# Kernel optimization log

Hardware: AMD Instinct MI355X
Metric: run time of the kernel (lower is better)

The kernel has to match this reference:

```python
import jax, jax.numpy as jnp
import numpy as np

NUM_HEADS = 16


def setup_inputs() -> dict:
    key = jax.random.key(0)
    ks = jax.random.split(key, 8)
    B, L, Hd = 2, 2048, 1024
    s = 0.02
    return {
        "x": jax.random.normal(ks[0], (B, L, Hd), jnp.float32),
        "y": jax.random.normal(ks[1], (B, L, Hd), jnp.float32),
        "mask": jnp.zeros((B, L), jnp.bool_),  # True = padding (masked out)
        "Wq_w": jax.random.normal(ks[2], (Hd, Hd), jnp.float32) * s,
        "Wq_b": jnp.zeros((Hd,), jnp.float32),
        "Wkv_w": jax.random.normal(ks[3], (Hd, 2 * Hd), jnp.float32) * s,
        "Wkv_b": jnp.zeros((2 * Hd,), jnp.float32),
        "proj_w": jax.random.normal(ks[4], (Hd, Hd), jnp.float32) * s,
        "proj_b": jnp.zeros((Hd,), jnp.float32),
    }


def reference(x, y, mask, Wq_w, Wq_b, Wkv_w, Wkv_b, proj_w, proj_b):
    B, L, Hd = x.shape
    H = NUM_HEADS
    D = Hd // H
    scale = 1.0 / np.sqrt(D)

    # projections (torch Linear: stored here already as (in, out))
    q = (x @ Wq_w + Wq_b).reshape(B, L, H, D).transpose(0, 2, 1, 3)   # bhld
    kv = (y @ Wkv_w + Wkv_b).reshape(B, L, 2, H, D)
    k = kv[:, :, 0].transpose(0, 2, 1, 3)                             # bhkd
    v = kv[:, :, 1].transpose(0, 2, 1, 3)                             # bhkd

    attn = jnp.einsum("bhld,bhkd->bhlk", q, k) * scale

    # combined padding (over keys) + causal mask; True = masked
    causal = jnp.triu(jnp.ones((L, L), jnp.bool_), 1)                 # (L, L)
    combined = mask[:, None, None, :] | causal[None, None]            # (B,1,L,L)
    attn = jnp.where(combined, -jnp.inf, attn)

    p = jax.nn.softmax(attn, axis=-1)
    out = jnp.einsum("bhlk,bhkd->bhld", p, v)
    out = out.transpose(0, 2, 1, 3).reshape(B, L, Hd)
    return out @ proj_w + proj_b
```

## Files before the change

kernel.cpp:

```cpp
#include <hip/hip_runtime.h>
#include <stdint.h>

#define B_  2
#define L_  2048
#define HD_ 1024
#define H_  16
#define D_  64

typedef unsigned short u16;
typedef __attribute__((ext_vector_type(8))) short bf16x8;
typedef __attribute__((ext_vector_type(4))) float f32x4;

#define MFMA16(a, b, c) __builtin_amdgcn_mfma_f32_16x16x32_bf16((a), (b), (c), 0, 0, 0)

__device__ __forceinline__ void gload16(const void* g, void* l) {
  __builtin_amdgcn_global_load_lds((const __attribute__((address_space(1))) void*)g,
                                   (__attribute__((address_space(3))) void*)l, 16, 0, 0);
}

__device__ __forceinline__ u16 f2bf(float f) {
  union { float f; uint32_t u; } c; c.f = f;
  uint32_t u = c.u + 0x7FFFu + ((c.u >> 16) & 1u);
  return (u16)(u >> 16);
}

__device__ __forceinline__ float bf2f(u16 v) {
  union { uint32_t u; float f; } c; c.u = (uint32_t)v << 16;
  return c.f;
}

__device__ __forceinline__ uint32_t cvt_pk_bf16(float lo, float hi) {
  uint32_t r;
  asm("v_cvt_pk_bf16_f32 %0, %1, %2" : "=v"(r) : "v"(lo), "v"(hi));
  return r;
}

__global__ void prologue_k(const float* __restrict__ x, const float* __restrict__ y,
                           u16* __restrict__ xb, u16* __restrict__ yb,
                           const float* __restrict__ Wq, const float* __restrict__ Wkv,
                           const float* __restrict__ Wp,
                           u16* __restrict__ Wqt, u16* __restrict__ Wkvt,
                           u16* __restrict__ Wpt) {
  int bid = blockIdx.x;
  int t = threadIdx.x;
  if (bid < 4096) {
    const float* in = bid < 2048 ? x : y;
    u16* out = bid < 2048 ? xb : yb;
    int i = ((bid & 2047) * 256 + t) * 8;
    float4 a = *(const float4*)(in + i);
    float4 b = *(const float4*)(in + i + 4);
    bf16x8 r;
    r[0] = (short)f2bf(a.x); r[1] = (short)f2bf(a.y); r[2] = (short)f2bf(a.z); r[3] = (short)f2bf(a.w);
    r[4] = (short)f2bf(b.x); r[5] = (short)f2bf(b.y); r[6] = (short)f2bf(b.z); r[7] = (short)f2bf(b.w);
    *(bf16x8*)(out + i) = r;
    return;
  }
  int f = bid - 4096;
  const float* src; u16* dst; int Nfull, bx, by;
  if (f < 1024)      { src = Wq;  dst = Wqt;  Nfull = 1024; bx = f & 31;  by = f >> 5; }
  else if (f < 3072) { int g2 = f - 1024; src = Wkv; dst = Wkvt; Nfull = 2048; bx = g2 & 63; by = g2 >> 6; }
  else               { int g2 = f - 3072; src = Wp;  dst = Wpt;  Nfull = 1024; bx = g2 & 31; by = g2 >> 5; }
  __shared__ float tile[32][33];
  int tc = t & 31, tr = t >> 5;
  int nb = bx * 32, kb = by * 32;
#pragma unroll
  for (int i = 0; i < 4; i++)
    tile[tr + i * 8][tc] = src[(size_t)(kb + tr + i * 8) * Nfull + nb + tc];
  __syncthreads();
#pragma unroll
  for (int i = 0; i < 4; i++) {
    int nl = tr + i * 8;
    dst[(size_t)(nb + nl) * 1024 + kb + tc] = f2bf(tile[tc][nl]);
  }
}

__device__ __forceinline__ void gemm64_body(
    char* sA, char* sB,
    const u16* __restrict__ A, const u16* __restrict__ Bt,
    const float* __restrict__ bias, void* __restrict__ outp,
    int N, int epi, int bm, int bn)
{
  int t = threadIdx.x;
  int lane = t & 63, w = t >> 6;
  int g = lane >> 4, l15 = lane & 15;
  int wr = w >> 1, wc = w & 1;

  f32x4 zero = {0.f, 0.f, 0.f, 0.f};
  f32x4 acc[2][4];
#pragma unroll
  for (int mi = 0; mi < 2; mi++)
#pragma unroll
    for (int ni = 0; ni < 4; ni++) acc[mi][ni] = zero;

#define GSTAGE64(bufi, k0s) do {                                                        \
    _Pragma("unroll")                                                                   \
    for (int it = 0; it < 2; it++) {             \
      int c = it * 256 + t;                                                             \
      int r = c >> 3, sp = c & 7;                                                       \
      int off = (sp ^ (r & 7)) << 4;                                                    \
      gload16((const char*)(A + (size_t)(bm + r) * 1024 + (k0s)) + off,                 \
              sA + (bufi) * 8192 + c * 16);                                             \
    }                                                                                   \
    _Pragma("unroll")                                                                   \
    for (int it = 0; it < 4; it++) {           \
      int c = it * 256 + t;                                                             \
      int r = c >> 3, sp = c & 7;                                                       \
      int off = (sp ^ (r & 7)) << 4;                                                    \
      gload16((const char*)(Bt + (size_t)(bn + r) * 1024 + (k0s)) + off,                \
              sB + (bufi) * 16384 + c * 16);                                            \
    } } while (0)

  GSTAGE64(0, 0);
  int buf = 0;
#pragma unroll 1
  for (int kt = 0; kt < 16; kt++) {
    __builtin_amdgcn_sched_barrier(0);
    __builtin_amdgcn_s_barrier();
    if (kt < 15) {
      GSTAGE64(buf ^ 1, (kt + 1) << 6);
      asm volatile("s_waitcnt vmcnt(6)" ::: "memory");
    } else {
      asm volatile("s_waitcnt vmcnt(0)" ::: "memory");
    }
    __builtin_amdgcn_s_barrier();
    __builtin_amdgcn_sched_barrier(0);

    const char* cA = sA + buf * 8192;
    const char* cB = sB + buf * 16384;
#pragma unroll
    for (int kc = 0; kc < 2; kc++) {
      bf16x8 af[2], bfr[4];
#pragma unroll
      for (int mi = 0; mi < 2; mi++) {
        int r = wr * 32 + mi * 16 + l15;
        af[mi] = *(const bf16x8*)(cA + r * 128 + (((kc * 4 + g) ^ (r & 7)) << 4));
      }
#pragma unroll
      for (int ni = 0; ni < 4; ni++) {
        int r = wc * 64 + ni * 16 + l15;
        bfr[ni] = *(const bf16x8*)(cB + r * 128 + (((kc * 4 + g) ^ (r & 7)) << 4));
      }
#pragma unroll
      for (int mi = 0; mi < 2; mi++)
#pragma unroll
        for (int ni = 0; ni < 4; ni++)
          acc[mi][ni] = MFMA16(af[mi], bfr[ni], acc[mi][ni]);
    }
    buf ^= 1;
  }
#undef GSTAGE64

  float bv[4];
#pragma unroll
  for (int ni = 0; ni < 4; ni++) bv[ni] = bias[bn + wc * 64 + ni * 16 + l15];

  if (epi == 2) {
    float* fo = (float*)outp;
#pragma unroll
    for (int mi = 0; mi < 2; mi++)
#pragma unroll
      for (int ni = 0; ni < 4; ni++) {
        int n = bn + wc * 64 + ni * 16 + l15;
#pragma unroll
        for (int r = 0; r < 4; r++) {
          int m = bm + wr * 32 + mi * 16 + g * 4 + r;
          fo[(size_t)m * N + n] = acc[mi][ni][r] + bv[ni];
        }
      }
  } else {
    const float QS = (epi == 0) ? 0.125f * 1.44269504089f : 1.0f;
    u16* ob = (u16*)outp;
#pragma unroll
    for (int mi = 0; mi < 2; mi++)
#pragma unroll
      for (int ni = 0; ni < 4; ni++) {
        int n = bn + wc * 64 + ni * 16 + l15;
        int kv = n >> 10;
        int hh = (n >> 6) & 15;
        int dd = n & 63;
        int m0 = bm + wr * 32 + mi * 16 + g * 4;
        int bb = m0 >> 11, lq0 = m0 & 2047;
        if (epi == 1 && kv == 1) {
          ushort4 pk;
          pk.x = f2bf(acc[mi][ni][0] + bv[ni]);
          pk.y = f2bf(acc[mi][ni][1] + bv[ni]);
          pk.z = f2bf(acc[mi][ni][2] + bv[ni]);
          pk.w = f2bf(acc[mi][ni][3] + bv[ni]);
          size_t idx = (size_t)(B_ * H_ * L_ * D_) +
                       (((size_t)(bb * H_ + hh) * D_ + dd) * L_ + lq0);
          *(ushort4*)(ob + idx) = pk;
        } else {
#pragma unroll
          for (int r = 0; r < 4; r++) {
            size_t idx = (((size_t)(bb * H_ + hh) * L_ + lq0 + r) * D_) + dd;
            ob[idx] = f2bf((acc[mi][ni][r] + bv[ni]) * QS);
          }
        }
      }
  }
}

__global__ __launch_bounds__(256, 3) void qkv_k(
    const u16* __restrict__ xb, const u16* __restrict__ yb,
    const u16* __restrict__ Wqt, const u16* __restrict__ Wkvt,
    const float* __restrict__ Wq_b, const float* __restrict__ Wkv_b,
    u16* __restrict__ Qout, u16* __restrict__ KVout)
{
  __shared__ char sA[2 * 8192];
  __shared__ char sB[2 * 16384];
  int bx = blockIdx.x, bm = blockIdx.y * 64;
  if (bx < 16)
    gemm64_body(sA, sB, yb, Wkvt, Wkv_b, (void*)KVout, 2048, 1, bm, bx * 128);
  else
    gemm64_body(sA, sB, xb, Wqt, Wq_b, (void*)Qout, 1024, 0, bm, (bx - 16) * 128);
}

__global__ __launch_bounds__(256, 3) void proj_k(
    const u16* __restrict__ A, const u16* __restrict__ Bt,
    const float* __restrict__ bias, float* __restrict__ fo)
{
  __shared__ char sA[2 * 8192];
  __shared__ char sB[2 * 16384];
  gemm64_body(sA, sB, A, Bt, bias, (void*)fo, 1024, 2,
              blockIdx.y * 64, blockIdx.x * 128);
}

__global__ __launch_bounds__(512, 2) void attn_k(
    const u16* __restrict__ Qb, const u16* __restrict__ Kb, const u16* __restrict__ Vt,
    const unsigned char* __restrict__ pad, u16* __restrict__ Ob,
    u16* __restrict__ Opart, float* __restrict__ mlbuf)
{
  __shared__ char sK[3][8192];
  __shared__ char sV[3][8192];
  __shared__ char sP[8][2048];
  int t = threadIdx.x, lane = t & 63, w = t >> 6, g = lane >> 4, l15 = lane & 15;
  int x = blockIdx.x, h = blockIdx.y, b = blockIdx.z, bh = b * H_ + h;
  int role = x >> 3, xp = x & 7;
  int qbH = 15 - xp, qbL = xp;
  int nktH = 2 * qbH + 2;
  const int SPLIT = 17;

  const u16* Kbh = Kb + (size_t)bh * L_ * D_;
  const u16* Vbh = Vt + (size_t)bh * D_ * L_;
  const unsigned char* pdb = pad + b * L_;
  int psw = l15 & 7;

  const uint4* pp = (const uint4*)pdb;
  uint4 pv0 = pp[lane];
  uint4 pv1 = pp[64 + lane];
  uint32_t nzp = pv0.x | pv0.y | pv0.z | pv0.w | pv1.x | pv1.y | pv1.z | pv1.w;
  bool anyp = __ballot(nzp != 0) != 0;

  int srr = t >> 3, ssp = t & 7;
  int sso = (ssp ^ (srr & 7)) << 4;
#define STAGE(bufi, kt0s) do {                                                        \
    gload16((const char*)(Kbh + (size_t)((kt0s) + srr) * D_) + sso, sK[bufi] + t * 16); \
    gload16((const char*)(Vbh + (size_t)srr * L_ + (kt0s)) + sso, sV[bufi] + t * 16);   \
  } while (0)

  int nphase = role ? 1 : 2;
#pragma unroll 1
  for (int ph = 0; ph < nphase; ph++) {
    int qb, lo, hi, mode;
    if (role) { qb = qbH; lo = 0;     hi = SPLIT;     mode = 1; }
    else if (ph == 0) { qb = qbL; lo = 0; hi = 2 * qbL + 2; mode = 0; }
    else { qb = qbH; lo = SPLIT; hi = nktH; mode = 2; }

    int qw0 = qb * 128 + w * 16;
    int bound = qw0 + 15;

    const u16* qp = Qb + ((size_t)bh * L_ + qw0 + l15) * D_ + g * 8;
    bf16x8 qf0 = *(const bf16x8*)qp;
    bf16x8 qf1 = *(const bf16x8*)(qp + 32);

    f32x4 zero = {0.f, 0.f, 0.f, 0.f};
    f32x4 oacc[4];
#pragma unroll
    for (int db = 0; db < 4; db++) oacc[db] = zero;
    float mrun = -1e30f, lrun = 0.f;

    if (ph) __syncthreads();
    STAGE(0, lo << 6);
    int cb = 0, nb = 1;

#pragma unroll 1
    for (int kt = lo; kt < hi; kt++) {
      int kt0 = kt << 6;
      __builtin_amdgcn_sched_barrier(0);
      if (kt + 1 < hi) {
        STAGE(nb, (kt + 1) << 6);
        asm volatile("s_waitcnt vmcnt(2)" ::: "memory");
      } else {
        asm volatile("s_waitcnt vmcnt(0)" ::: "memory");
      }
      __builtin_amdgcn_s_barrier();
      __builtin_amdgcn_sched_barrier(0);

      if (kt0 <= bound) {
        float sc[4][4];
#pragma unroll
        for (int s = 0; s < 4; s++) {
          int kb = kt0 + s * 16;
          bool live = (kb <= bound);
          f32x4 st = zero;
          uint32_t pb = 0;
          if (live) {
            int R = s * 16 + l15, sw = l15 & 7;
            bf16x8 kf0 = *(const bf16x8*)(sK[cb] + R * 128 + ((g ^ sw) << 4));
            bf16x8 kf1 = *(const bf16x8*)(sK[cb] + R * 128 + (((4 + g) ^ sw) << 4));
            st = MFMA16(kf0, qf0, st);
            st = MFMA16(kf1, qf1, st);
            if (anyp) pb = *(const uint32_t*)(pdb + kb + 4 * g);
          }
          bool needm = !live || (kb + 15 > qw0) || anyp;
          if (needm) {
#pragma unroll
            for (int r = 0; r < 4; r++) {
              int key = kb + 4 * g + r;
              bool pm = (pb >> (8 * r)) & 0xffu;
              bool msk = !live || pm || (key > qw0 + l15);
              sc[s][r] = msk ? -1e30f : st[r];
            }
          } else {
#pragma unroll
            for (int r = 0; r < 4; r++) sc[s][r] = st[r];
          }
        }

        float m0 = fmaxf(fmaxf(sc[0][0], sc[0][1]), fmaxf(sc[0][2], sc[0][3]));
        float m1 = fmaxf(fmaxf(sc[1][0], sc[1][1]), fmaxf(sc[1][2], sc[1][3]));
        float m2 = fmaxf(fmaxf(sc[2][0], sc[2][1]), fmaxf(sc[2][2], sc[2][3]));
        float m3 = fmaxf(fmaxf(sc[3][0], sc[3][1]), fmaxf(sc[3][2], sc[3][3]));
        float mt = fmaxf(fmaxf(m0, m1), fmaxf(m2, m3));
        mt = fmaxf(mt, __shfl_xor(mt, 16));
        mt = fmaxf(mt, __shfl_xor(mt, 32));
        if (!__all(mt <= mrun + 8.0f)) {
          float mnew = fmaxf(mrun, mt);
          float al = __builtin_amdgcn_exp2f(mrun - mnew);
          mrun = mnew;
          lrun *= al;
#pragma unroll
          for (int db = 0; db < 4; db++)
#pragma unroll
            for (int r = 0; r < 4; r++) oacc[db][r] *= al;
        }
        float rs = 0.f;
        char* pwb = sP[w] + l15 * 128 + (g & 1) * 8;
#pragma unroll
        for (int s = 0; s < 4; s++) {
          float p0 = __builtin_amdgcn_exp2f(sc[s][0] - mrun);
          float p1 = __builtin_amdgcn_exp2f(sc[s][1] - mrun);
          float p2 = __builtin_amdgcn_exp2f(sc[s][2] - mrun);
          float p3 = __builtin_amdgcn_exp2f(sc[s][3] - mrun);
          rs += (p0 + p1) + (p2 + p3);
          uint32_t w0 = cvt_pk_bf16(p0, p1), w1 = cvt_pk_bf16(p2, p3);
          char* dst = pwb + (((2 * s + (g >> 1)) ^ psw) << 4);
          *(uint32_t*)dst = w0;
          *(uint32_t*)(dst + 4) = w1;
        }
        rs += __shfl_xor(rs, 16);
        rs += __shfl_xor(rs, 32);
        lrun += rs;

#pragma unroll
        for (int kc = 0; kc < 2; kc++) {
          if (kt0 + 32 * kc <= bound) {
            bf16x8 pf = *(const bf16x8*)(sP[w] + l15 * 128 + (((4 * kc + g) ^ psw) << 4));
#pragma unroll
            for (int db = 0; db < 4; db++) {
              int dR = db * 16 + l15;
              bf16x8 vf = *(const bf16x8*)(sV[cb] + dR * 128 +
                                           (((4 * kc + g) ^ (dR & 7)) << 4));
              oacc[db] = MFMA16(vf, pf, oacc[db]);
            }
          }
        }
      }
      cb = (cb == 2) ? 0 : cb + 1;
      nb = (nb == 2) ? 0 : nb + 1;
    }

    float rl = (lrun != 0.f) ? 1.0f / lrun : 0.f;
    int q = qw0 + l15;
    if (mode == 0) {
      u16* op = Ob + ((size_t)b * L_ + q) * HD_ + h * D_ + g * 4;
#pragma unroll
      for (int db = 0; db < 4; db++) {
        ushort4 pk;
        pk.x = f2bf(oacc[db][0] * rl);
        pk.y = f2bf(oacc[db][1] * rl);
        pk.z = f2bf(oacc[db][2] * rl);
        pk.w = f2bf(oacc[db][3] * rl);
        *(ushort4*)(op + db * 16) = pk;
      }
    } else {
      int part = mode - 1;
      size_t prow = (size_t)part * 32768 + (size_t)bh * 1024 + (q - 1024);
      u16* op = Opart + prow * 64 + g * 4;
#pragma unroll
      for (int db = 0; db < 4; db++) {
        ushort4 pk;
        pk.x = f2bf(oacc[db][0] * rl);
        pk.y = f2bf(oacc[db][1] * rl);
        pk.z = f2bf(oacc[db][2] * rl);
        pk.w = f2bf(oacc[db][3] * rl);
        *(ushort4*)(op + db * 16) = pk;
      }
      if (g == 0) {
        mlbuf[prow * 2]     = mrun;
        mlbuf[prow * 2 + 1] = lrun;
      }
    }
  }
#undef STAGE
}

__global__ __launch_bounds__(256) void merge_k(
    const u16* __restrict__ Op, const float* __restrict__ ml, u16* __restrict__ Ob)
{
  int tid = blockIdx.x * 256 + threadIdx.x;
  int d0 = (tid & 7) * 8;
  int row = tid >> 3;
  int qrel = row & 1023, bh = row >> 10;
  int b = bh >> 4, h = bh & 15;
  float m0 = ml[(size_t)row * 2],            l0 = ml[(size_t)row * 2 + 1];
  float m1 = ml[((size_t)32768 + row) * 2],  l1 = ml[((size_t)32768 + row) * 2 + 1];
  float M = fmaxf(m0, m1);
  float w0 = l0 * __builtin_amdgcn_exp2f(m0 - M);
  float w1 = l1 * __builtin_amdgcn_exp2f(m1 - M);
  float rw = 1.0f / (w0 + w1);
  w0 *= rw; w1 *= rw;
  bf16x8 a = *(const bf16x8*)(Op + (size_t)row * 64 + d0);
  bf16x8 c = *(const bf16x8*)(Op + ((size_t)32768 + row) * 64 + d0);
  bf16x8 o;
#pragma unroll
  for (int j = 0; j < 8; j++)
    o[j] = (short)f2bf(w0 * bf2f((u16)a[j]) + w1 * bf2f((u16)c[j]));
  *(bf16x8*)(Ob + ((size_t)b * L_ + 1024 + qrel) * HD_ + h * D_ + d0) = o;
}

extern "C" void kernel_launch(void* const* d_in, const int* in_sizes, int n_in,
                              void* d_out, int out_size, void* d_ws, size_t ws_size,
                              hipStream_t stream) {
  const float* x      = (const float*)d_in[0];
  const float* y      = (const float*)d_in[1];
  const unsigned char* mask = (const unsigned char*)d_in[2];
  const float* Wq_w   = (const float*)d_in[3];
  const float* Wq_b   = (const float*)d_in[4];
  const float* Wkv_w  = (const float*)d_in[5];
  const float* Wkv_b  = (const float*)d_in[6];
  const float* proj_w = (const float*)d_in[7];
  const float* proj_b = (const float*)d_in[8];

  char* ws = (char*)d_ws;
  u16* xb   = (u16*)(ws);
  u16* yb   = (u16*)(ws + (size_t)(8  << 20));
  u16* Wqt  = (u16*)(ws + (size_t)(16 << 20));
  u16* Wkvt = (u16*)(ws + (size_t)(18 << 20));
  u16* Wpt  = (u16*)(ws + (size_t)(22 << 20));
  u16* Qb   = (u16*)(ws + (size_t)(24 << 20));
  u16* Kb   = (u16*)(ws + (size_t)(32 << 20));
  u16* Vtb  = (u16*)(ws + (size_t)(40 << 20));
  u16* Ob   = xb;
  u16* Opart  = yb;
  float* mlbuf = (float*)Wqt;

  hipLaunchKernelGGL(prologue_k, dim3(8192), dim3(256), 0, stream,
                     x, y, xb, yb, Wq_w, Wkv_w, proj_w, Wqt, Wkvt, Wpt);
  hipLaunchKernelGGL(qkv_k, dim3(24, 64), dim3(256), 0, stream,
                     xb, yb, Wqt, Wkvt, Wq_b, Wkv_b, Qb, Kb);
  hipLaunchKernelGGL(attn_k, dim3(16, H_, B_), dim3(512), 0, stream,
                     Qb, Kb, Vtb, mask, Ob, Opart, mlbuf);
  hipLaunchKernelGGL(merge_k, dim3(1024), dim3(256), 0, stream, Opart, mlbuf, Ob);
  hipLaunchKernelGGL(proj_k, dim3(8, 64), dim3(256), 0, stream, Ob, Wpt, proj_b, (float*)d_out);
}
```

Baseline: 114.6 us.

## Fuse attention phases into one pipelined loop and widen weight transpose tiles

The attention kernel's two-phase loop (low q-block, then high q-block tail) becomes a single 17-iteration stream of K/V tiles. The prefetch pipeline therefore continues across the phase boundary, with an in-loop switch that writes the first output and reloads Q. This removes the pipeline drain, the extra barrier and the restaging at the phase change. Separately, the weight transpose in the prologue moves to 64x64 tiles with float4 loads and ushort4 stores, cutting the block count and widening memory accesses, at the cost of more shared memory per block.

```diff
diff --git a/kernel.cpp b/kernel.cpp
--- a/kernel.cpp
+++ b/kernel.cpp
@@ -57,20 +57,30 @@
   }
   int f = bid - 4096;
   const float* src; u16* dst; int Nfull, bx, by;
-  if (f < 1024)      { src = Wq;  dst = Wqt;  Nfull = 1024; bx = f & 31;  by = f >> 5; }
-  else if (f < 3072) { int g2 = f - 1024; src = Wkv; dst = Wkvt; Nfull = 2048; bx = g2 & 63; by = g2 >> 6; }
-  else               { int g2 = f - 3072; src = Wp;  dst = Wpt;  Nfull = 1024; bx = g2 & 31; by = g2 >> 5; }
-  __shared__ float tile[32][33];
-  int tc = t & 31, tr = t >> 5;
-  int nb = bx * 32, kb = by * 32;
-#pragma unroll
-  for (int i = 0; i < 4; i++)
-    tile[tr + i * 8][tc] = src[(size_t)(kb + tr + i * 8) * Nfull + nb + tc];
+  if (f < 256)      { src = Wq;  dst = Wqt;  Nfull = 1024; bx = f & 15;  by = f >> 4; }
+  else if (f < 768) { int g2 = f - 256; src = Wkv; dst = Wkvt; Nfull = 2048; bx = g2 & 31; by = g2 >> 5; }
+  else              { int g2 = f - 768; src = Wp;  dst = Wpt;  Nfull = 1024; bx = g2 & 15; by = g2 >> 4; }
+  __shared__ float tile[64][65];
+  int c = t & 15, r = t >> 4;
+  int nb = bx * 64, kb = by * 64;
+#pragma unroll
+  for (int i = 0; i < 4; i++) {
+    float4 v = *(const float4*)(src + (size_t)(kb + r + i * 16) * Nfull + nb + c * 4);
+    tile[r + i * 16][c * 4 + 0] = v.x;
+    tile[r + i * 16][c * 4 + 1] = v.y;
+    tile[r + i * 16][c * 4 + 2] = v.z;
+    tile[r + i * 16][c * 4 + 3] = v.w;
+  }
   __syncthreads();
 #pragma unroll
   for (int i = 0; i < 4; i++) {
-    int nl = tr + i * 8;
-    dst[(size_t)(nb + nl) * 1024 + kb + tc] = f2bf(tile[tc][nl]);
+    int nl = r + i * 16;
+    ushort4 o;
+    o.x = f2bf(tile[c * 4 + 0][nl]);
+    o.y = f2bf(tile[c * 4 + 1][nl]);
+    o.z = f2bf(tile[c * 4 + 2][nl]);
+    o.w = f2bf(tile[c * 4 + 3][nl]);
+    *(ushort4*)(dst + (size_t)(nb + nl) * 1024 + kb + c * 4) = o;
   }
 }
 
@@ -237,8 +247,9 @@
   int x = blockIdx.x, h = blockIdx.y, b = blockIdx.z, bh = b * H_ + h;
   int role = x >> 3, xp = x & 7;
   int qbH = 15 - xp, qbL = xp;
-  int nktH = 2 * qbH + 2;
   const int SPLIT = 17;
+  int nL = 2 * qbL + 2;
+  int boundary = role ? 99 : nL;
 
   const u16* Kbh = Kb + (size_t)bh * L_ * D_;
   const u16* Vbh = Vt + (size_t)bh * D_ * L_;
@@ -257,162 +268,166 @@
     gload16((const char*)(Kbh + (size_t)((kt0s) + srr) * D_) + sso, sK[bufi] + t * 16); \
     gload16((const char*)(Vbh + (size_t)srr * L_ + (kt0s)) + sso, sV[bufi] + t * 16);   \
   } while (0)
-
-  int nphase = role ? 1 : 2;
+#define KT0_OF(jj) ((role ? (jj) : ((jj) < nL ? (jj) : SPLIT + (jj) - nL)) << 6)
+
+  int qb_cur = role ? qbH : qbL;
+  int qw0 = qb_cur * 128 + w * 16;
+  int bound = qw0 + 15;
+
+  const u16* qp = Qb + ((size_t)bh * L_ + qw0 + l15) * D_ + g * 8;
+  bf16x8 qf0 = *(const bf16x8*)qp;
+  bf16x8 qf1 = *(const bf16x8*)(qp + 32);
+
+  f32x4 zero = {0.f, 0.f, 0.f, 0.f};
+  f32x4 oacc[4];
+#pragma unroll
+  for (int db = 0; db < 4; db++) oacc[db] = zero;
+  float mrun = -1e30f, lrun = 0.f;
+
+  STAGE(0, 0);
+  int cb = 0, nb = 1;
+
 #pragma unroll 1
-  for (int ph = 0; ph < nphase; ph++) {
-    int qb, lo, hi, mode;
-    if (role) { qb = qbH; lo = 0;     hi = SPLIT;     mode = 1; }
-    else if (ph == 0) { qb = qbL; lo = 0; hi = 2 * qbL + 2; mode = 0; }
-    else { qb = qbH; lo = SPLIT; hi = nktH; mode = 2; }
-
-    int qw0 = qb * 128 + w * 16;
-    int bound = qw0 + 15;
-
-    const u16* qp = Qb + ((size_t)bh * L_ + qw0 + l15) * D_ + g * 8;
-    bf16x8 qf0 = *(const bf16x8*)qp;
-    bf16x8 qf1 = *(const bf16x8*)(qp + 32);
-
-    f32x4 zero = {0.f, 0.f, 0.f, 0.f};
-    f32x4 oacc[4];
-#pragma unroll
-    for (int db = 0; db < 4; db++) oacc[db] = zero;
-    float mrun = -1e30f, lrun = 0.f;
-
-    if (ph) __syncthreads();
-    STAGE(0, lo << 6);
-    int cb = 0, nb = 1;
-
-#pragma unroll 1
-    for (int kt = lo; kt < hi; kt++) {
-      int kt0 = kt << 6;
-      __builtin_amdgcn_sched_barrier(0);
-      if (kt + 1 < hi) {
-        STAGE(nb, (kt + 1) << 6);
-        asm volatile("s_waitcnt vmcnt(2)" ::: "memory");
-      } else {
-        asm volatile("s_waitcnt vmcnt(0)" ::: "memory");
-      }
-      __builtin_amdgcn_s_barrier();
-      __builtin_amdgcn_sched_barrier(0);
-
-      if (kt0 <= bound) {
-        float sc[4][4];
-#pragma unroll
-        for (int s = 0; s < 4; s++) {
-          int kb = kt0 + s * 16;
-          bool live = (kb <= bound);
-          f32x4 st = zero;
-          uint32_t pb = 0;
-          if (live) {
-            int R = s * 16 + l15, sw = l15 & 7;
-            bf16x8 kf0 = *(const bf16x8*)(sK[cb] + R * 128 + ((g ^ sw) << 4));
-            bf16x8 kf1 = *(const bf16x8*)(sK[cb] + R * 128 + (((4 + g) ^ sw) << 4));
-            st = MFMA16(kf0, qf0, st);
-            st = MFMA16(kf1, qf1, st);
-            if (anyp) pb = *(const uint32_t*)(pdb + kb + 4 * g);
+  for (int j = 0; j < 17; j++) {
+    __builtin_amdgcn_sched_barrier(0);
+    if (j + 1 < 17) {
+      STAGE(nb, KT0_OF(j + 1));
+      asm volatile("s_waitcnt vmcnt(2)" ::: "memory");
+    } else {
+      asm volatile("s_waitcnt vmcnt(0)" ::: "memory");
+    }
+    __builtin_amdgcn_s_barrier();
+    __builtin_amdgcn_sched_barrier(0);
+
+    if (j == boundary) {
+      float rl0 = (lrun != 0.f) ? 1.0f / lrun : 0.f;
+      int q0 = qw0 + l15;
+      u16* op0 = Ob + ((size_t)b * L_ + q0) * HD_ + h * D_ + g * 4;
+#pragma unroll
+      for (int db = 0; db < 4; db++) {
+        ushort4 pk;
+        pk.x = f2bf(oacc[db][0] * rl0);
+        pk.y = f2bf(oacc[db][1] * rl0);
+        pk.z = f2bf(oacc[db][2] * rl0);
+        pk.w = f2bf(oacc[db][3] * rl0);
+        *(ushort4*)(op0 + db * 16) = pk;
+      }
+      qb_cur = qbH;
+      qw0 = qb_cur * 128 + w * 16;
+      bound = qw0 + 15;
+      const u16* qp2 = Qb + ((size_t)bh * L_ + qw0 + l15) * D_ + g * 8;
+      qf0 = *(const bf16x8*)qp2;
+      qf1 = *(const bf16x8*)(qp2 + 32);
+#pragma unroll
+      for (int db = 0; db < 4; db++) oacc[db] = zero;
+      mrun = -1e30f; lrun = 0.f;
+    }
+
+    int kt0 = KT0_OF(j);
+    if (kt0 <= bound) {
+      float sc[4][4];
+#pragma unroll
+      for (int s = 0; s < 4; s++) {
+        int kb = kt0 + s * 16;
+        bool live = (kb <= bound);
+        f32x4 st = zero;
+        uint32_t pb = 0;
+        if (live) {
+          int R = s * 16 + l15, sw = l15 & 7;
+          bf16x8 kf0 = *(const bf16x8*)(sK[cb] + R * 128 + ((g ^ sw) << 4));
+          bf16x8 kf1 = *(const bf16x8*)(sK[cb] + R * 128 + (((4 + g) ^ sw) << 4));
+          st = MFMA16(kf0, qf0, st);
+          st = MFMA16(kf1, qf1, st);
+          if (anyp) pb = *(const uint32_t*)(pdb + kb + 4 * g);
+        }
+        bool needm = !live || (kb + 15 > qw0) || anyp;
+        if (needm) {
+#pragma unroll
+          for (int r = 0; r < 4; r++) {
+            int key = kb + 4 * g + r;
+            bool pm = (pb >> (8 * r)) & 0xffu;
+            bool msk = !live || pm || (key > qw0 + l15);
+            sc[s][r] = msk ? -1e30f : st[r];
           }
-          bool needm = !live || (kb + 15 > qw0) || anyp;
-          if (needm) {
-#pragma unroll
-            for (int r = 0; r < 4; r++) {
-              int key = kb + 4 * g + r;
-              bool pm = (pb >> (8 * r)) & 0xffu;
-              bool msk = !live || pm || (key > qw0 + l15);
-              sc[s][r] = msk ? -1e30f : st[r];
-            }
-          } else {
-#pragma unroll
-            for (int r = 0; r < 4; r++) sc[s][r] = st[r];
+        } else {
+#pragma unroll
+          for (int r = 0; r < 4; r++) sc[s][r] = st[r];
+        }
+      }
+
+      float m0 = fmaxf(fmaxf(sc[0][0], sc[0][1]), fmaxf(sc[0][2], sc[0][3]));
+      float m1 = fmaxf(fmaxf(sc[1][0], sc[1][1]), fmaxf(sc[1][2], sc[1][3]));
+      float m2 = fmaxf(fmaxf(sc[2][0], sc[2][1]), fmaxf(sc[2][2], sc[2][3]));
+      float m3 = fmaxf(fmaxf(sc[3][0], sc[3][1]), fmaxf(sc[3][2], sc[3][3]));
+      float mt = fmaxf(fmaxf(m0, m1), fmaxf(m2, m3));
+      mt = fmaxf(mt, __shfl_xor(mt, 16));
+      mt = fmaxf(mt, __shfl_xor(mt, 32));
+      if (!__all(mt <= mrun + 8.0f)) {
+        float mnew = fmaxf(mrun, mt);
+        float al = __builtin_amdgcn_exp2f(mrun - mnew);
+        mrun = mnew;
+        lrun *= al;
+#pragma unroll
+        for (int db = 0; db < 4; db++)
+#pragma unroll
+          for (int r = 0; r < 4; r++) oacc[db][r] *= al;
+      }
+      float rs = 0.f;
+      char* pwb = sP[w] + l15 * 128 + (g & 1) * 8;
+#pragma unroll
+      for (int s = 0; s < 4; s++) {
+        float p0 = __builtin_amdgcn_exp2f(sc[s][0] - mrun);
+        float p1 = __builtin_amdgcn_exp2f(sc[s][1] - mrun);
+        float p2 = __builtin_amdgcn_exp2f(sc[s][2] - mrun);
+        float p3 = __builtin_amdgcn_exp2f(sc[s][3] - mrun);
+        rs += (p0 + p1) + (p2 + p3);
+        uint32_t w0 = cvt_pk_bf16(p0, p1), w1 = cvt_pk_bf16(p2, p3);
+        char* dst = pwb + (((2 * s + (g >> 1)) ^ psw) << 4);
+        *(uint32_t*)dst = w0;
+        *(uint32_t*)(dst + 4) = w1;
+      }
+      rs += __shfl_xor(rs, 16);
+      rs += __shfl_xor(rs, 32);
+      lrun += rs;
+
+#pragma unroll
+      for (int kc = 0; kc < 2; kc++) {
+        if (kt0 + 32 * kc <= bound) {
+          bf16x8 pf = *(const bf16x8*)(sP[w] + l15 * 128 + (((4 * kc + g) ^ psw) << 4));
+#pragma unroll
+          for (int db = 0; db < 4; db++) {
+            int dR = db * 16 + l15;
+            bf16x8 vf = *(const bf16x8*)(sV[cb] + dR * 128 +
+                                         (((4 * kc + g) ^ (dR & 7)) << 4));
+            oacc[db] = MFMA16(vf, pf, oacc[db]);
           }
         }
-
-        float m0 = fmaxf(fmaxf(sc[0][0], sc[0][1]), fmaxf(sc[0][2], sc[0][3]));
-        float m1 = fmaxf(fmaxf(sc[1][0], sc[1][1]), fmaxf(sc[1][2], sc[1][3]));
-        float m2 = fmaxf(fmaxf(sc[2][0], sc[2][1]), fmaxf(sc[2][2], sc[2][3]));
-        float m3 = fmaxf(fmaxf(sc[3][0], sc[3][1]), fmaxf(sc[3][2], sc[3][3]));
-        float mt = fmaxf(fmaxf(m0, m1), fmaxf(m2, m3));
-        mt = fmaxf(mt, __shfl_xor(mt, 16));
-        mt = fmaxf(mt, __shfl_xor(mt, 32));
-        if (!__all(mt <= mrun + 8.0f)) {
-          float mnew = fmaxf(mrun, mt);
-          float al = __builtin_amdgcn_exp2f(mrun - mnew);
-          mrun = mnew;
-          lrun *= al;
-#pragma unroll
-          for (int db = 0; db < 4; db++)
-#pragma unroll
-            for (int r = 0; r < 4; r++) oacc[db][r] *= al;
-        }
-        float rs = 0.f;
-        char* pwb = sP[w] + l15 * 128 + (g & 1) * 8;
-#pragma unroll
-        for (int s = 0; s < 4; s++) {
-          float p0 = __builtin_amdgcn_exp2f(sc[s][0] - mrun);
-          float p1 = __builtin_amdgcn_exp2f(sc[s][1] - mrun);
-          float p2 = __builtin_amdgcn_exp2f(sc[s][2] - mrun);
-          float p3 = __builtin_amdgcn_exp2f(sc[s][3] - mrun);
-          rs += (p0 + p1) + (p2 + p3);
-          uint32_t w0 = cvt_pk_bf16(p0, p1), w1 = cvt_pk_bf16(p2, p3);
-          char* dst = pwb + (((2 * s + (g >> 1)) ^ psw) << 4);
-          *(uint32_t*)dst = w0;
-          *(uint32_t*)(dst + 4) = w1;
-        }
-        rs += __shfl_xor(rs, 16);
-        rs += __shfl_xor(rs, 32);
-        lrun += rs;
-
-#pragma unroll
-        for (int kc = 0; kc < 2; kc++) {
-          if (kt0 + 32 * kc <= bound) {
-            bf16x8 pf = *(const bf16x8*)(sP[w] + l15 * 128 + (((4 * kc + g) ^ psw) << 4));
-#pragma unroll
-            for (int db = 0; db < 4; db++) {
-              int dR = db * 16 + l15;
-              bf16x8 vf = *(const bf16x8*)(sV[cb] + dR * 128 +
-                                           (((4 * kc + g) ^ (dR & 7)) << 4));
-              oacc[db] = MFMA16(vf, pf, oacc[db]);
-            }
-          }
-        }
-      }
-      cb = (cb == 2) ? 0 : cb + 1;
-      nb = (nb == 2) ? 0 : nb + 1;
+      }
     }
-
-    float rl = (lrun != 0.f) ? 1.0f / lrun : 0.f;
-    int q = qw0 + l15;
-    if (mode == 0) {
-      u16* op = Ob + ((size_t)b * L_ + q) * HD_ + h * D_ + g * 4;
-#pragma unroll
-      for (int db = 0; db < 4; db++) {
-        ushort4 pk;
-        pk.x = f2bf(oacc[db][0] * rl);
-        pk.y = f2bf(oacc[db][1] * rl);
-        pk.z = f2bf(oacc[db][2] * rl);
-        pk.w = f2bf(oacc[db][3] * rl);
-        *(ushort4*)(op + db * 16) = pk;
-      }
-    } else {
-      int part = mode - 1;
-      size_t prow = (size_t)part * 32768 + (size_t)bh * 1024 + (q - 1024);
-      u16* op = Opart + prow * 64 + g * 4;
-#pragma unroll
-      for (int db = 0; db < 4; db++) {
-        ushort4 pk;
-        pk.x = f2bf(oacc[db][0] * rl);
-        pk.y = f2bf(oacc[db][1] * rl);
-        pk.z = f2bf(oacc[db][2] * rl);
-        pk.w = f2bf(oacc[db][3] * rl);
-        *(ushort4*)(op + db * 16) = pk;
-      }
-      if (g == 0) {
-        mlbuf[prow * 2]     = mrun;
-        mlbuf[prow * 2 + 1] = lrun;
-      }
-    }
+    cb = (cb == 2) ? 0 : cb + 1;
+    nb = (nb == 2) ? 0 : nb + 1;
+  }
+
+  float rl = (lrun != 0.f) ? 1.0f / lrun : 0.f;
+  int q = qw0 + l15;
+  int part = role ? 0 : 1;
+  size_t prow = (size_t)part * 32768 + (size_t)bh * 1024 + (q - 1024);
+  u16* op = Opart + prow * 64 + g * 4;
+#pragma unroll
+  for (int db = 0; db < 4; db++) {
+    ushort4 pk;
+    pk.x = f2bf(oacc[db][0] * rl);
+    pk.y = f2bf(oacc[db][1] * rl);
+    pk.z = f2bf(oacc[db][2] * rl);
+    pk.w = f2bf(oacc[db][3] * rl);
+    *(ushort4*)(op + db * 16) = pk;
+  }
+  if (g == 0) {
+    mlbuf[prow * 2]     = mrun;
+    mlbuf[prow * 2 + 1] = lrun;
   }
 #undef STAGE
+#undef KT0_OF
 }
 
 __global__ __launch_bounds__(256) void merge_k(
@@ -465,7 +480,7 @@
   u16* Opart  = yb;
   float* mlbuf = (float*)Wqt;
 
-  hipLaunchKernelGGL(prologue_k, dim3(8192), dim3(256), 0, stream,
+  hipLaunchKernelGGL(prologue_k, dim3(5120), dim3(256), 0, stream,
                      x, y, xb, yb, Wq_w, Wkv_w, proj_w, Wqt, Wkvt, Wpt);
   hipLaunchKernelGGL(qkv_k, dim3(24, 64), dim3(256), 0, stream,
                      xb, yb, Wqt, Wkvt, Wq_b, Wkv_b, Qb, Kb);
```

After: 116.4 us. Within noise of the previous version (+1.6%).
